# Performance work log

Measured on AMD Instinct MI355X. Metric: run time of the kernel, lower is better.

Reference implementation:

```python
import jax, jax.numpy as jnp
import numpy as np

B, N, H = 32, 2048, 128


def _lstm_step(c, h, x, Wi, Wh, b):
    # flax LSTMCell: gates i,f,g,o; sigmoid/sigmoid/tanh/sigmoid
    gates = x @ Wi + h @ Wh + b  # (B,N,4H)
    i, f, g, o = jnp.split(gates, 4, axis=-1)
    c_new = jax.nn.sigmoid(f) * c + jax.nn.sigmoid(i) * jnp.tanh(g)
    h_new = jax.nn.sigmoid(o) * jnp.tanh(c_new)
    return c_new, h_new


def setup_inputs() -> dict:
    key = jax.random.key(0)
    ks = jax.random.split(key, 24)
    f32 = jnp.float32
    inp = {}
    inp['node_embeddings'] = jax.random.normal(ks[0], (B, N, H), f32)
    for nm, k in zip(['hs_c0', 'hs_h0', 'hs_c1', 'hs_h1'], ks[1:5]):
        inp[nm] = jax.random.normal(k, (B, N, H), f32)
    ip = jax.random.uniform(ks[5], (B, N), f32)
    inp['instruction_pointer'] = ip / jnp.sum(ip, axis=-1, keepdims=True)
    inp['Wi0'] = jax.random.normal(ks[6], (H, 4 * H), f32) * 0.05
    inp['Wh0'] = jax.random.normal(ks[7], (H, 4 * H), f32) * 0.05
    inp['b0'] = jnp.zeros((4 * H,), f32)
    inp['Wi1'] = jax.random.normal(ks[8], (H, 4 * H), f32) * 0.05
    inp['Wh1'] = jax.random.normal(ks[9], (H, 4 * H), f32) * 0.05
    inp['b1'] = jnp.zeros((4 * H,), f32)
    inp['W_raise'] = jax.random.normal(ks[10], (4 * H, 2), f32) * 0.05
    inp['b_raise'] = jnp.zeros((2,), f32)
    inp['W_branch'] = jax.random.normal(ks[11], (4 * H, 2), f32) * 0.05
    inp['b_branch'] = jnp.zeros((2,), f32)
    inp['true_indexes'] = jax.random.randint(ks[12], (B, N), 0, N, jnp.int32)
    inp['false_indexes'] = jax.random.randint(ks[13], (B, N), 0, N, jnp.int32)
    inp['raise_indexes'] = jax.random.randint(ks[14], (B, N), 0, N, jnp.int32)
    inp['exit_node_indexes'] = jax.random.randint(ks[15], (B,), 0, N, jnp.int32)
    inp['raise_node_indexes'] = jax.random.randint(ks[16], (B,), 0, N, jnp.int32)
    inp['step_limits'] = jax.random.randint(ks[17], (B,), 0, 100, jnp.int32)
    inp['current_step'] = 5
    return inp


def reference(node_embeddings, hs_c0, hs_h0, hs_c1, hs_h1, instruction_pointer,
              Wi0, Wh0, b0, Wi1, Wh1, b1, W_raise, b_raise, W_branch, b_branch,
              true_indexes, false_indexes, raise_indexes,
              exit_node_indexes, raise_node_indexes, step_limits, current_step):
    bidx = jnp.arange(B)
    old = [hs_c0, hs_h0, hs_c1, hs_h1]

    # execute: per-node 2-layer stacked LSTM (vectorized over B,N)
    c0n, h0n = _lstm_step(hs_c0, hs_h0, node_embeddings, Wi0, Wh0, b0)
    c1n, h1n = _lstm_step(hs_c1, hs_h1, h0n, Wi1, Wh1, b1)
    contrib = [c0n, h0n, c1n, h1n]

    # mask_h: keep old state at exit node and (raise_in_ipagnn) at raise node
    def mask_nodes(hc, ho, idx):
        return hc.at[bidx, idx].set(ho[bidx, idx])
    contrib = [mask_nodes(mask_nodes(hc, ho, exit_node_indexes), ho, raise_node_indexes)
               for hc, ho in zip(contrib, old)]

    hs_emb = jnp.concatenate(contrib, axis=-1)  # (B,N,4H)

    raise_dec = jax.nn.softmax(hs_emb @ W_raise + b_raise, axis=-1)
    zero_one = jnp.array([0.0, 1.0], dtype=raise_dec.dtype)
    raise_dec = raise_dec.at[bidx, exit_node_indexes].set(zero_one)
    raise_dec = raise_dec.at[bidx, raise_node_indexes].set(zero_one)
    branch_dec = jax.nn.softmax(hs_emb @ W_branch + b_branch, axis=-1)

    p_raise = raise_dec[..., 0]
    p_noraise = raise_dec[..., 1]
    p_true = p_noraise * branch_dec[..., 0]
    p_false = p_noraise * branch_dec[..., 1]

    seg = jax.vmap(lambda v, idx: jax.ops.segment_sum(v, idx, num_segments=N))
    ip = instruction_pointer
    ip_new = (seg(p_raise * ip, raise_indexes)
              + seg(p_true * ip, true_indexes)
              + seg(p_false * ip, false_indexes))  # (B,N)
    denom = (ip_new + 1e-7)[..., None]

    wr = (p_raise * ip)[..., None]
    wt = (p_true * ip)[..., None]
    wf = (p_false * ip)[..., None]

    def agg(h):
        return (seg(h * wr, raise_indexes) + seg(h * wt, true_indexes)
                + seg(h * wf, false_indexes)) / denom
    hs_new = [agg(h) for h in contrib]

    # keep_old_if_done
    not_done = (current_step < step_limits)  # (B,)
    hs_out = [jnp.where(not_done[:, None, None], hn, ho) for hn, ho in zip(hs_new, old)]
    ip_out = jnp.where(not_done[:, None], ip_new, ip)

    # pack carry: (c0,h0,c1,h1, instruction_pointer) -> (B,N,4H+1)
    return jnp.concatenate(hs_out + [ip_out[..., None]], axis=-1)
```

## Files before the change

### kernel.cpp

```cpp
#include <hip/hip_runtime.h>
#include <stdint.h>

#define BB 32
#define NN 2048
#define HH 128
#define BN (BB*NN)

typedef short v8s __attribute__((ext_vector_type(8)));
typedef float v4f __attribute__((ext_vector_type(4)));

__device__ __forceinline__ unsigned short f2b(float f){
  union { float f; unsigned int i; } v; v.f = f;
  unsigned int x = v.i;
  unsigned int r = x + 0x7FFFu + ((x >> 16) & 1u);
  return (unsigned short)(r >> 16);
}
__device__ __forceinline__ unsigned int pk2(float a, float b){
  return (unsigned int)f2b(a) | ((unsigned int)f2b(b) << 16);
}
__device__ __forceinline__ float frcp(float x){ return __builtin_amdgcn_rcpf(x); }
__device__ __forceinline__ float fsigm(float x){ return frcp(1.0f + __expf(-x)); }
__device__ __forceinline__ float ftanh(float x){ return 1.0f - 2.0f*frcp(1.0f + __expf(2.0f*x)); }

__global__ void kswz(const float* __restrict__ Wi0, const float* __restrict__ Wh0,
                     const float* __restrict__ Wi1, const float* __restrict__ Wh1,
                     unsigned short* __restrict__ Bsw0, unsigned short* __restrict__ Bsw1){
  int bid = blockIdx.x;
  int layer = bid >> 8;
  int kc = (bid >> 5) & 7;
  int ct = bid & 31;
  int lane = threadIdx.x;
  const float* Wi = layer ? Wi1 : Wi0;
  const float* Wh = layer ? Wh1 : Wh0;
  unsigned short* dst = layer ? Bsw1 : Bsw0;
  int col = ct*16 + (lane & 15);
  int kbase = kc*32 + (lane >> 4)*8;
  size_t o = ((size_t)(kc*32 + ct)*64 + (size_t)lane)*8;
  #pragma unroll
  for (int j = 0; j < 8; j++){
    int k = kbase + j;
    dst[o + j] = f2b((k < 128) ? Wi[k*512 + col] : Wh[(k-128)*512 + col]);
  }
}

__global__ void ksave(const float* __restrict__ c0, const float* __restrict__ h0,
                      const float* __restrict__ c1, const float* __restrict__ h1,
                      const int* __restrict__ exit_idx, const int* __restrict__ raise_idx,
                      float* __restrict__ saved){
  int b = blockIdx.x, which = blockIdx.y, c = threadIdx.x;
  int idx = which ? raise_idx[b] : exit_idx[b];
  size_t row = (size_t)b*NN + idx;
  const float* bufs[4] = {c0, h0, c1, h1};
  saved[((size_t)b*2 + which)*512 + c] = bufs[c >> 7][row*128 + (c & 127)];
}

__global__ void krestore(float* c0, float* h0, float* c1, float* h1,
                         const int* __restrict__ exit_idx, const int* __restrict__ raise_idx,
                         const float* __restrict__ saved){
  int b = blockIdx.x, which = blockIdx.y, c = threadIdx.x;
  int idx = which ? raise_idx[b] : exit_idx[b];
  size_t row = (size_t)b*NN + idx;
  float* bufs[4] = {c0, h0, c1, h1};
  bufs[c >> 7][row*128 + (c & 127)] = saved[((size_t)b*2 + which)*512 + c];
}

#define ROWSB 32
#define PA 264
#define PH 136

__global__ __launch_bounds__(512, 4) void klstm2(
    const float* __restrict__ ne,
    float* __restrict__ c0, float* __restrict__ h0,
    float* __restrict__ c1, float* __restrict__ h1,
    const unsigned short* __restrict__ Bsw0, const float* __restrict__ b0,
    const unsigned short* __restrict__ Bsw1, const float* __restrict__ b1,
    const int* __restrict__ step_limits, const int* __restrict__ cur_step)
{
  __shared__ unsigned short ldsA[ROWSB*PA];
  __shared__ unsigned short ldsH[ROWSB*PH];
  __shared__ unsigned short ldsG[ROWSB*PH];

  int rowbase = blockIdx.x * ROWSB;
  int b = rowbase >> 11;
  if (cur_step[0] >= step_limits[b]) return;

  int tid = threadIdx.x;
  int wid = tid >> 6, lane = tid & 63;
  int quad = lane >> 4, l16 = lane & 15;
  int ch = wid*16 + l16;

  #pragma unroll
  for (int p = 0; p < 4; p++){
    int idx = p*512 + tid;
    int row = idx >> 6, chunk = idx & 63;
    size_t g = (size_t)(rowbase + row)*128 + (chunk & 31)*4;
    float4 v = (chunk < 32) ? *(const float4*)(ne + g) : *(const float4*)(h0 + g);
    uint2 w; w.x = pk2(v.x, v.y); w.y = pk2(v.z, v.w);
    *(uint2*)&ldsA[row*PA + chunk*4] = w;
  }
  __syncthreads();

  float cpre[8], bias[4];
  #pragma unroll
  for (int rt = 0; rt < 2; rt++)
    #pragma unroll
    for (int r = 0; r < 4; r++)
      cpre[rt*4+r] = c0[((size_t)rowbase + rt*16 + quad*4 + r)*128 + ch];
  #pragma unroll
  for (int g = 0; g < 4; g++) bias[g] = b0[g*128 + ch];

  #pragma unroll
  for (int p = 0; p < 2; p++){
    int idx = p*512 + tid;
    int row = idx >> 5, chunk = idx & 31;
    float4 v = *(const float4*)(h1 + (size_t)(rowbase + row)*128 + chunk*4);
    uint2 w; w.x = pk2(v.x, v.y); w.y = pk2(v.z, v.w);
    *(uint2*)&ldsH[row*PH + chunk*4] = w;
  }

  const v8s* Bv0 = (const v8s*)Bsw0;
  v4f acc[2][4] = {};
  v8s bc[4], bn[4];
  #pragma unroll
  for (int g = 0; g < 4; g++) bc[g] = Bv0[(size_t)(g*8 + wid)*64 + lane];
  #pragma unroll
  for (int kc = 0; kc < 8; kc++){
    if (kc < 7){
      #pragma unroll
      for (int g = 0; g < 4; g++) bn[g] = Bv0[(size_t)((kc+1)*32 + g*8 + wid)*64 + lane];
    }
    v8s a0 = *(const v8s*)&ldsA[(0*16 + l16)*PA + kc*32 + quad*8];
    v8s a1 = *(const v8s*)&ldsA[(1*16 + l16)*PA + kc*32 + quad*8];
    #pragma unroll
    for (int g = 0; g < 4; g++){
      acc[0][g] = __builtin_amdgcn_mfma_f32_16x16x32_bf16(a0, bc[g], acc[0][g], 0,0,0);
      acc[1][g] = __builtin_amdgcn_mfma_f32_16x16x32_bf16(a1, bc[g], acc[1][g], 0,0,0);
    }
    #pragma unroll
    for (int g = 0; g < 4; g++) bc[g] = bn[g];
  }

  #pragma unroll
  for (int rt = 0; rt < 2; rt++){
    #pragma unroll
    for (int r = 0; r < 4; r++){
      int lrow = rt*16 + quad*4 + r;
      size_t row = (size_t)rowbase + lrow;
      float iv = acc[rt][0][r] + bias[0];
      float fv = acc[rt][1][r] + bias[1];
      float gv = acc[rt][2][r] + bias[2];
      float ov = acc[rt][3][r] + bias[3];
      float cold = cpre[rt*4+r];
      float cn = fsigm(fv)*cold + fsigm(iv)*ftanh(gv);
      float hn = fsigm(ov)*ftanh(cn);
      c0[row*128 + ch] = cn;
      h0[row*128 + ch] = hn;
      ldsG[lrow*PH + ch] = f2b(hn);
    }
  }
  __syncthreads();

  #pragma unroll
  for (int rt = 0; rt < 2; rt++)
    #pragma unroll
    for (int r = 0; r < 4; r++)
      cpre[rt*4+r] = c1[((size_t)rowbase + rt*16 + quad*4 + r)*128 + ch];
  #pragma unroll
  for (int g = 0; g < 4; g++) bias[g] = b1[g*128 + ch];

  const v8s* Bv1 = (const v8s*)Bsw1;
  #pragma unroll
  for (int rt = 0; rt < 2; rt++)
    #pragma unroll
    for (int g = 0; g < 4; g++)
      acc[rt][g] = (v4f){0.f, 0.f, 0.f, 0.f};
  #pragma unroll
  for (int g = 0; g < 4; g++) bc[g] = Bv1[(size_t)(g*8 + wid)*64 + lane];
  #pragma unroll
  for (int kc = 0; kc < 8; kc++){
    if (kc < 7){
      #pragma unroll
      for (int g = 0; g < 4; g++) bn[g] = Bv1[(size_t)((kc+1)*32 + g*8 + wid)*64 + lane];
    }
    v8s a0, a1;
    if (kc < 4){
      a0 = *(const v8s*)&ldsG[(0*16 + l16)*PH + kc*32 + quad*8];
      a1 = *(const v8s*)&ldsG[(1*16 + l16)*PH + kc*32 + quad*8];
    } else {
      a0 = *(const v8s*)&ldsH[(0*16 + l16)*PH + (kc-4)*32 + quad*8];
      a1 = *(const v8s*)&ldsH[(1*16 + l16)*PH + (kc-4)*32 + quad*8];
    }
    #pragma unroll
    for (int g = 0; g < 4; g++){
      acc[0][g] = __builtin_amdgcn_mfma_f32_16x16x32_bf16(a0, bc[g], acc[0][g], 0,0,0);
      acc[1][g] = __builtin_amdgcn_mfma_f32_16x16x32_bf16(a1, bc[g], acc[1][g], 0,0,0);
    }
    #pragma unroll
    for (int g = 0; g < 4; g++) bc[g] = bn[g];
  }

  #pragma unroll
  for (int rt = 0; rt < 2; rt++){
    #pragma unroll
    for (int r = 0; r < 4; r++){
      size_t row = (size_t)rowbase + rt*16 + quad*4 + r;
      float iv = acc[rt][0][r] + bias[0];
      float fv = acc[rt][1][r] + bias[1];
      float gv = acc[rt][2][r] + bias[2];
      float ov = acc[rt][3][r] + bias[3];
      float cold = cpre[rt*4+r];
      float cn = fsigm(fv)*cold + fsigm(iv)*ftanh(gv);
      float hn = fsigm(ov)*ftanh(cn);
      c1[row*128 + ch] = cn;
      h1[row*128 + ch] = hn;
    }
  }
}

__global__ __launch_bounds__(256) void kdec(
    const float* __restrict__ c0, const float* __restrict__ h0,
    const float* __restrict__ c1, const float* __restrict__ h1,
    const float* __restrict__ Wr, const float* __restrict__ br,
    const float* __restrict__ Wb, const float* __restrict__ bb,
    const float* __restrict__ ip,
    const int* __restrict__ exit_idx, const int* __restrict__ raise_idx,
    const int* __restrict__ ri, const int* __restrict__ ti, const int* __restrict__ fi,
    int* __restrict__ counts,
    float* __restrict__ wbuf)
{
  int tid = threadIdx.x;
  int wid = tid >> 6, lane = tid & 63;
  int gid = blockIdx.x*4 + wid;
  int b = gid >> 11, n = gid & 2047;

  const float* bufs[4] = {c0, h0, c1, h1};
  const float* hb = bufs[lane >> 4] + (size_t)gid*128 + (lane & 15)*8;
  float4 hv0 = *(const float4*)hb;
  float4 hv1 = *(const float4*)(hb + 4);
  float hv[8] = {hv0.x, hv0.y, hv0.z, hv0.w, hv1.x, hv1.y, hv1.z, hv1.w};
  const float* wrp = Wr + lane*16;
  const float* wbp = Wb + lane*16;
  float r0=0.f, r1=0.f, q0=0.f, q1=0.f;
  #pragma unroll
  for (int j = 0; j < 8; j++){
    float h = hv[j];
    r0 += h * wrp[j*2];  r1 += h * wrp[j*2+1];
    q0 += h * wbp[j*2];  q1 += h * wbp[j*2+1];
  }
  #pragma unroll
  for (int off = 32; off > 0; off >>= 1){
    r0 += __shfl_xor(r0, off, 64);
    r1 += __shfl_xor(r1, off, 64);
    q0 += __shfl_xor(q0, off, 64);
    q1 += __shfl_xor(q1, off, 64);
  }
  if (lane == 0){
    r0 += br[0]; r1 += br[1];
    q0 += bb[0]; q1 += bb[1];
    float pr, pn;
    if (n == exit_idx[b] || n == raise_idx[b]){ pr = 0.f; pn = 1.f; }
    else {
      float m = fmaxf(r0, r1);
      float e0 = __expf(r0 - m), e1 = __expf(r1 - m);
      pr = e0 / (e0 + e1); pn = e1 / (e0 + e1);
    }
    float m2 = fmaxf(q0, q1);
    float f0 = __expf(q0 - m2), f1 = __expf(q1 - m2);
    float pt = f0 / (f0 + f1), pf = f1 / (f0 + f1);
    float ipv = ip[gid];
    wbuf[0*BN + gid] = pr * ipv;
    wbuf[1*BN + gid] = pn * pt * ipv;
    wbuf[2*BN + gid] = pn * pf * ipv;
  } else if (lane == 1){
    atomicAdd(&counts[(b<<11) + ri[gid]], 1);
  } else if (lane == 2){
    atomicAdd(&counts[(b<<11) + ti[gid]], 1);
  } else if (lane == 3){
    atomicAdd(&counts[(b<<11) + fi[gid]], 1);
  }
}

__global__ __launch_bounds__(256) void kscan(const int* __restrict__ counts,
                                             int* __restrict__ offsets){
  __shared__ int lds[256];
  int b = blockIdx.x, tid = threadIdx.x;
  const int* c = counts + b*NN;
  int* o = offsets + b*NN;
  int v[8]; int s = 0;
  #pragma unroll
  for (int i = 0; i < 8; i++){ v[i] = c[tid*8+i]; s += v[i]; }
  lds[tid] = s;
  __syncthreads();
  if (tid == 0){
    int run = 0;
    for (int t = 0; t < 256; t++){ int tmp = lds[t]; lds[t] = run; run += tmp; }
  }
  __syncthreads();
  int off = lds[tid];
  #pragma unroll
  for (int i = 0; i < 8; i++){ o[tid*8+i] = off; off += v[i]; }
}

__global__ void kfill(const int* __restrict__ ri, const int* __restrict__ ti,
                      const int* __restrict__ fi, const int* __restrict__ offsets,
                      int* __restrict__ cursor, unsigned short* __restrict__ edges){
  int gid = blockIdx.x*256 + threadIdx.x;
  int b = gid >> 11, n = gid & 2047;
  size_t ebase = (size_t)b*3*NN;
  int t0 = ri[gid]; int p0 = atomicAdd(&cursor[b*NN+t0], 1);
  edges[ebase + offsets[b*NN+t0] + p0] = (unsigned short)(n);
  int t1 = ti[gid]; int p1 = atomicAdd(&cursor[b*NN+t1], 1);
  edges[ebase + offsets[b*NN+t1] + p1] = (unsigned short)(n | (1<<11));
  int t2 = fi[gid]; int p2 = atomicAdd(&cursor[b*NN+t2], 1);
  edges[ebase + offsets[b*NN+t2] + p2] = (unsigned short)(n | (2<<11));
}

__global__ __launch_bounds__(128) void kagg(
    const float* __restrict__ c0, const float* __restrict__ h0,
    const float* __restrict__ c1, const float* __restrict__ h1,
    const float* __restrict__ ip,
    const float* __restrict__ wbuf, const unsigned short* __restrict__ edges,
    const int* __restrict__ counts, const int* __restrict__ offsets,
    const int* __restrict__ step_limits, const int* __restrict__ cur_step,
    float* __restrict__ out)
{
  int gid = blockIdx.x;
  int b = gid >> 11;
  int tid = threadIdx.x;
  size_t obase = (size_t)gid*513;
  const float* bufs[4] = {c0, h0, c1, h1};

  if (cur_step[0] >= step_limits[b]){
    int c = tid*4;
    const float* s = bufs[c >> 7];
    size_t rb = (size_t)gid*128 + (c & 127);
    out[obase + c+0] = s[rb+0];
    out[obase + c+1] = s[rb+1];
    out[obase + c+2] = s[rb+2];
    out[obase + c+3] = s[rb+3];
    if (tid == 0) out[obase + 512] = ip[gid];
    return;
  }

  int cnt = counts[gid], off = offsets[gid];
  const unsigned short* eb = edges + (size_t)b*3*NN + off;
  const float* sb = bufs[tid >> 5];
  int coff = (tid & 31)*4;
  float a0=0.f, a1=0.f, a2=0.f, a3=0.f, ipn=0.f;
  for (int e = 0; e < cnt; e++){
    int pk = eb[e];
    int n = pk & 2047, et = pk >> 11;
    float w = wbuf[et*BN + (b<<11) + n];
    ipn += w;
    float4 sv = *(const float4*)(sb + ((size_t)(b<<11) + n)*128 + coff);
    a0 += w * sv.x;
    a1 += w * sv.y;
    a2 += w * sv.z;
    a3 += w * sv.w;
  }
  int c = tid*4;
  float inv = 1.0f / (ipn + 1e-7f);
  out[obase + c+0] = a0*inv;
  out[obase + c+1] = a1*inv;
  out[obase + c+2] = a2*inv;
  out[obase + c+3] = a3*inv;
  if (tid == 0) out[obase + 512] = ipn;
}

extern "C" void kernel_launch(void* const* d_in, const int* in_sizes, int n_in,
                              void* d_out, int out_size, void* d_ws, size_t ws_size,
                              hipStream_t stream){
  const float* ne  = (const float*)d_in[0];
  float* c0  = (float*)d_in[1];
  float* h0  = (float*)d_in[2];
  float* c1  = (float*)d_in[3];
  float* h1  = (float*)d_in[4];
  const float* ip  = (const float*)d_in[5];
  const float* Wi0 = (const float*)d_in[6];
  const float* Wh0 = (const float*)d_in[7];
  const float* b0  = (const float*)d_in[8];
  const float* Wi1 = (const float*)d_in[9];
  const float* Wh1 = (const float*)d_in[10];
  const float* b1  = (const float*)d_in[11];
  const float* Wr  = (const float*)d_in[12];
  const float* br  = (const float*)d_in[13];
  const float* Wb  = (const float*)d_in[14];
  const float* bb  = (const float*)d_in[15];
  const int* ti  = (const int*)d_in[16];
  const int* fi  = (const int*)d_in[17];
  const int* ri  = (const int*)d_in[18];
  const int* ei  = (const int*)d_in[19];
  const int* rni = (const int*)d_in[20];
  const int* sl  = (const int*)d_in[21];
  const int* cs  = (const int*)d_in[22];
  float* out = (float*)d_out;

  uint8_t* ws = (uint8_t*)d_ws;
  unsigned short* Bsw0    = (unsigned short*)(ws + 0);
  unsigned short* Bsw1    = (unsigned short*)(ws + 262144);
  float*          saved   = (float*)(ws + 524288);
  float*          wbuf    = (float*)(ws + 655360);
  int*            counts  = (int*)(ws + 1441792);
  int*            offsets = (int*)(ws + 1703936);
  int*            cursor  = (int*)(ws + 1966080);
  unsigned short* edges   = (unsigned short*)(ws + 2228224);

  hipMemsetAsync(counts, 0, BN*sizeof(int), stream);
  hipMemsetAsync(cursor, 0, BN*sizeof(int), stream);

  kswz<<<512, 64, 0, stream>>>(Wi0, Wh0, Wi1, Wh1, Bsw0, Bsw1);
  ksave<<<dim3(BB, 2), 512, 0, stream>>>(c0, h0, c1, h1, ei, rni, saved);

  klstm2<<<BN/ROWSB, 512, 0, stream>>>(ne, c0, h0, c1, h1, Bsw0, b0, Bsw1, b1, sl, cs);

  krestore<<<dim3(BB, 2), 512, 0, stream>>>(c0, h0, c1, h1, ei, rni, saved);

  kdec<<<BN/4, 256, 0, stream>>>(c0, h0, c1, h1, Wr, br, Wb, bb, ip, ei, rni,
                                 ri, ti, fi, counts, wbuf);

  kscan<<<BB, 256, 0, stream>>>(counts, offsets);
  kfill<<<BN/256, 256, 0, stream>>>(ri, ti, fi, offsets, cursor, edges);

  kagg<<<BN, 128, 0, stream>>>(c0, h0, c1, h1, ip, wbuf, edges, counts, offsets,
                               sl, cs, out);
}
```

Baseline: 463.5 us.

## Make LSTM kernel persistent with double-buffered prefetch; drop save/restore kernels and memset

The LSTM kernel becomes a persistent grid of 512 blocks that loops over row tiles. While the current tile computes, it prefetches the next tile's inputs into registers and double-buffered LDS. The exit and raise rows are now skipped in the write-back, so the separate save and restore kernels can be removed. The cursor memset is folded into the scan kernel, and the aggregation loop prefetches the next edge index. This cuts launch count and global-load latency, at the cost of more LDS per block (lower occupancy) and weight fragments reloaded each k-step without the earlier register pipelining.

```diff
diff --git a/kernel.cpp b/kernel.cpp
--- a/kernel.cpp
+++ b/kernel.cpp
@@ -43,28 +43,9 @@
   }
 }
 
-__global__ void ksave(const float* __restrict__ c0, const float* __restrict__ h0,
-                      const float* __restrict__ c1, const float* __restrict__ h1,
-                      const int* __restrict__ exit_idx, const int* __restrict__ raise_idx,
-                      float* __restrict__ saved){
-  int b = blockIdx.x, which = blockIdx.y, c = threadIdx.x;
-  int idx = which ? raise_idx[b] : exit_idx[b];
-  size_t row = (size_t)b*NN + idx;
-  const float* bufs[4] = {c0, h0, c1, h1};
-  saved[((size_t)b*2 + which)*512 + c] = bufs[c >> 7][row*128 + (c & 127)];
-}
-
-__global__ void krestore(float* c0, float* h0, float* c1, float* h1,
-                         const int* __restrict__ exit_idx, const int* __restrict__ raise_idx,
-                         const float* __restrict__ saved){
-  int b = blockIdx.x, which = blockIdx.y, c = threadIdx.x;
-  int idx = which ? raise_idx[b] : exit_idx[b];
-  size_t row = (size_t)b*NN + idx;
-  float* bufs[4] = {c0, h0, c1, h1};
-  bufs[c >> 7][row*128 + (c & 127)] = saved[((size_t)b*2 + which)*512 + c];
-}
-
 #define ROWSB 32
+#define NTILES (BN/ROWSB)
+#define GRID 512
 #define PA 264
 #define PH 136
 
@@ -74,146 +55,205 @@
     float* __restrict__ c1, float* __restrict__ h1,
     const unsigned short* __restrict__ Bsw0, const float* __restrict__ b0,
     const unsigned short* __restrict__ Bsw1, const float* __restrict__ b1,
+    const int* __restrict__ exit_idx, const int* __restrict__ raise_idx,
     const int* __restrict__ step_limits, const int* __restrict__ cur_step)
 {
-  __shared__ unsigned short ldsA[ROWSB*PA];
-  __shared__ unsigned short ldsH[ROWSB*PH];
+  __shared__ unsigned short ldsA[2][ROWSB*PA];
+  __shared__ unsigned short ldsH[2][ROWSB*PH];
   __shared__ unsigned short ldsG[ROWSB*PH];
-
-  int rowbase = blockIdx.x * ROWSB;
-  int b = rowbase >> 11;
-  if (cur_step[0] >= step_limits[b]) return;
 
   int tid = threadIdx.x;
   int wid = tid >> 6, lane = tid & 63;
   int quad = lane >> 4, l16 = lane & 15;
   int ch = wid*16 + l16;
-
-  #pragma unroll
-  for (int p = 0; p < 4; p++){
-    int idx = p*512 + tid;
-    int row = idx >> 6, chunk = idx & 63;
-    size_t g = (size_t)(rowbase + row)*128 + (chunk & 31)*4;
-    float4 v = (chunk < 32) ? *(const float4*)(ne + g) : *(const float4*)(h0 + g);
-    uint2 w; w.x = pk2(v.x, v.y); w.y = pk2(v.z, v.w);
-    *(uint2*)&ldsA[row*PA + chunk*4] = w;
+  int curstep = cur_step[0];
+
+  int arow[4], achk[4], hrow[2], hchk[2];
+  #pragma unroll
+  for (int p = 0; p < 4; p++){ int idx = p*512 + tid; arow[p] = idx >> 6; achk[p] = idx & 63; }
+  #pragma unroll
+  for (int p = 0; p < 2; p++){ int idx = p*512 + tid; hrow[p] = idx >> 5; hchk[p] = idx & 31; }
+
+  const v8s* Bv0 = (const v8s*)Bsw0;
+  const v8s* Bv1 = (const v8s*)Bsw1;
+
+  float4 rgA[4], rgH[2];
+
+  int t0 = blockIdx.x;
+  if (curstep < step_limits[t0 >> 6]){
+    int rowbase = t0 * ROWSB;
+    #pragma unroll
+    for (int p = 0; p < 4; p++){
+      size_t g = (size_t)(rowbase + arow[p])*128 + (achk[p] & 31)*4;
+      rgA[p] = (achk[p] < 32) ? *(const float4*)(ne + g) : *(const float4*)(h0 + g);
+    }
+    #pragma unroll
+    for (int p = 0; p < 2; p++)
+      rgH[p] = *(const float4*)(h1 + (size_t)(rowbase + hrow[p])*128 + hchk[p]*4);
+    #pragma unroll
+    for (int p = 0; p < 4; p++){
+      uint2 w; w.x = pk2(rgA[p].x, rgA[p].y); w.y = pk2(rgA[p].z, rgA[p].w);
+      *(uint2*)&ldsA[0][arow[p]*PA + achk[p]*4] = w;
+    }
+    #pragma unroll
+    for (int p = 0; p < 2; p++){
+      uint2 w; w.x = pk2(rgH[p].x, rgH[p].y); w.y = pk2(rgH[p].z, rgH[p].w);
+      *(uint2*)&ldsH[0][hrow[p]*PH + hchk[p]*4] = w;
+    }
   }
   __syncthreads();
 
-  float cpre[8], bias[4];
-  #pragma unroll
-  for (int rt = 0; rt < 2; rt++)
-    #pragma unroll
-    for (int r = 0; r < 4; r++)
-      cpre[rt*4+r] = c0[((size_t)rowbase + rt*16 + quad*4 + r)*128 + ch];
-  #pragma unroll
-  for (int g = 0; g < 4; g++) bias[g] = b0[g*128 + ch];
-
-  #pragma unroll
-  for (int p = 0; p < 2; p++){
-    int idx = p*512 + tid;
-    int row = idx >> 5, chunk = idx & 31;
-    float4 v = *(const float4*)(h1 + (size_t)(rowbase + row)*128 + chunk*4);
-    uint2 w; w.x = pk2(v.x, v.y); w.y = pk2(v.z, v.w);
-    *(uint2*)&ldsH[row*PH + chunk*4] = w;
-  }
-
-  const v8s* Bv0 = (const v8s*)Bsw0;
-  v4f acc[2][4] = {};
-  v8s bc[4], bn[4];
-  #pragma unroll
-  for (int g = 0; g < 4; g++) bc[g] = Bv0[(size_t)(g*8 + wid)*64 + lane];
-  #pragma unroll
-  for (int kc = 0; kc < 8; kc++){
-    if (kc < 7){
-      #pragma unroll
-      for (int g = 0; g < 4; g++) bn[g] = Bv0[(size_t)((kc+1)*32 + g*8 + wid)*64 + lane];
-    }
-    v8s a0 = *(const v8s*)&ldsA[(0*16 + l16)*PA + kc*32 + quad*8];
-    v8s a1 = *(const v8s*)&ldsA[(1*16 + l16)*PA + kc*32 + quad*8];
-    #pragma unroll
-    for (int g = 0; g < 4; g++){
-      acc[0][g] = __builtin_amdgcn_mfma_f32_16x16x32_bf16(a0, bc[g], acc[0][g], 0,0,0);
-      acc[1][g] = __builtin_amdgcn_mfma_f32_16x16x32_bf16(a1, bc[g], acc[1][g], 0,0,0);
-    }
-    #pragma unroll
-    for (int g = 0; g < 4; g++) bc[g] = bn[g];
-  }
-
-  #pragma unroll
-  for (int rt = 0; rt < 2; rt++){
-    #pragma unroll
-    for (int r = 0; r < 4; r++){
-      int lrow = rt*16 + quad*4 + r;
-      size_t row = (size_t)rowbase + lrow;
-      float iv = acc[rt][0][r] + bias[0];
-      float fv = acc[rt][1][r] + bias[1];
-      float gv = acc[rt][2][r] + bias[2];
-      float ov = acc[rt][3][r] + bias[3];
-      float cold = cpre[rt*4+r];
-      float cn = fsigm(fv)*cold + fsigm(iv)*ftanh(gv);
-      float hn = fsigm(ov)*ftanh(cn);
-      c0[row*128 + ch] = cn;
-      h0[row*128 + ch] = hn;
-      ldsG[lrow*PH + ch] = f2b(hn);
-    }
-  }
-  __syncthreads();
-
-  #pragma unroll
-  for (int rt = 0; rt < 2; rt++)
-    #pragma unroll
-    for (int r = 0; r < 4; r++)
-      cpre[rt*4+r] = c1[((size_t)rowbase + rt*16 + quad*4 + r)*128 + ch];
-  #pragma unroll
-  for (int g = 0; g < 4; g++) bias[g] = b1[g*128 + ch];
-
-  const v8s* Bv1 = (const v8s*)Bsw1;
-  #pragma unroll
-  for (int rt = 0; rt < 2; rt++)
-    #pragma unroll
-    for (int g = 0; g < 4; g++)
-      acc[rt][g] = (v4f){0.f, 0.f, 0.f, 0.f};
-  #pragma unroll
-  for (int g = 0; g < 4; g++) bc[g] = Bv1[(size_t)(g*8 + wid)*64 + lane];
-  #pragma unroll
-  for (int kc = 0; kc < 8; kc++){
-    if (kc < 7){
-      #pragma unroll
-      for (int g = 0; g < 4; g++) bn[g] = Bv1[(size_t)((kc+1)*32 + g*8 + wid)*64 + lane];
-    }
-    v8s a0, a1;
-    if (kc < 4){
-      a0 = *(const v8s*)&ldsG[(0*16 + l16)*PH + kc*32 + quad*8];
-      a1 = *(const v8s*)&ldsG[(1*16 + l16)*PH + kc*32 + quad*8];
-    } else {
-      a0 = *(const v8s*)&ldsH[(0*16 + l16)*PH + (kc-4)*32 + quad*8];
-      a1 = *(const v8s*)&ldsH[(1*16 + l16)*PH + (kc-4)*32 + quad*8];
-    }
-    #pragma unroll
-    for (int g = 0; g < 4; g++){
-      acc[0][g] = __builtin_amdgcn_mfma_f32_16x16x32_bf16(a0, bc[g], acc[0][g], 0,0,0);
-      acc[1][g] = __builtin_amdgcn_mfma_f32_16x16x32_bf16(a1, bc[g], acc[1][g], 0,0,0);
-    }
-    #pragma unroll
-    for (int g = 0; g < 4; g++) bc[g] = bn[g];
-  }
-
-  #pragma unroll
-  for (int rt = 0; rt < 2; rt++){
-    #pragma unroll
-    for (int r = 0; r < 4; r++){
-      size_t row = (size_t)rowbase + rt*16 + quad*4 + r;
-      float iv = acc[rt][0][r] + bias[0];
-      float fv = acc[rt][1][r] + bias[1];
-      float gv = acc[rt][2][r] + bias[2];
-      float ov = acc[rt][3][r] + bias[3];
-      float cold = cpre[rt*4+r];
-      float cn = fsigm(fv)*cold + fsigm(iv)*ftanh(gv);
-      float hn = fsigm(ov)*ftanh(cn);
-      c1[row*128 + ch] = cn;
-      h1[row*128 + ch] = hn;
-    }
+  int cur = 0;
+  for (int t = t0; t < NTILES; t += GRID){
+    int tn = t + GRID;
+    bool alive_c = (curstep < step_limits[t >> 6]);
+    bool alive_n = (tn < NTILES) && (curstep < step_limits[tn >> 6]);
+    int rowbase = t * ROWSB;
+    int b = rowbase >> 11;
+
+    if (alive_n){
+      int rb2 = tn * ROWSB;
+      #pragma unroll
+      for (int p = 0; p < 4; p++){
+        size_t g = (size_t)(rb2 + arow[p])*128 + (achk[p] & 31)*4;
+        rgA[p] = (achk[p] < 32) ? *(const float4*)(ne + g) : *(const float4*)(h0 + g);
+      }
+      #pragma unroll
+      for (int p = 0; p < 2; p++)
+        rgH[p] = *(const float4*)(h1 + (size_t)(rb2 + hrow[p])*128 + hchk[p]*4);
+    }
+
+    v4f acc[2][4] = {};
+    float cpre[8], bias[4];
+    int e_row = 0, r_row = 0;
+
+    if (alive_c){
+      e_row = exit_idx[b]; r_row = raise_idx[b];
+      #pragma unroll
+      for (int rt = 0; rt < 2; rt++)
+        #pragma unroll
+        for (int r = 0; r < 4; r++)
+          cpre[rt*4+r] = c0[((size_t)rowbase + rt*16 + quad*4 + r)*128 + ch];
+      #pragma unroll
+      for (int g = 0; g < 4; g++) bias[g] = b0[g*128 + ch];
+
+      #pragma unroll
+      for (int kc = 0; kc < 8; kc++){
+        v8s f0 = Bv0[(size_t)(kc*32 + 0*8 + wid)*64 + lane];
+        v8s f1 = Bv0[(size_t)(kc*32 + 1*8 + wid)*64 + lane];
+        v8s f2 = Bv0[(size_t)(kc*32 + 2*8 + wid)*64 + lane];
+        v8s f3 = Bv0[(size_t)(kc*32 + 3*8 + wid)*64 + lane];
+        v8s a0 = *(const v8s*)&ldsA[cur][(0*16 + l16)*PA + kc*32 + quad*8];
+        v8s a1 = *(const v8s*)&ldsA[cur][(1*16 + l16)*PA + kc*32 + quad*8];
+        acc[0][0] = __builtin_amdgcn_mfma_f32_16x16x32_bf16(a0, f0, acc[0][0], 0,0,0);
+        acc[1][0] = __builtin_amdgcn_mfma_f32_16x16x32_bf16(a1, f0, acc[1][0], 0,0,0);
+        acc[0][1] = __builtin_amdgcn_mfma_f32_16x16x32_bf16(a0, f1, acc[0][1], 0,0,0);
+        acc[1][1] = __builtin_amdgcn_mfma_f32_16x16x32_bf16(a1, f1, acc[1][1], 0,0,0);
+        acc[0][2] = __builtin_amdgcn_mfma_f32_16x16x32_bf16(a0, f2, acc[0][2], 0,0,0);
+        acc[1][2] = __builtin_amdgcn_mfma_f32_16x16x32_bf16(a1, f2, acc[1][2], 0,0,0);
+        acc[0][3] = __builtin_amdgcn_mfma_f32_16x16x32_bf16(a0, f3, acc[0][3], 0,0,0);
+        acc[1][3] = __builtin_amdgcn_mfma_f32_16x16x32_bf16(a1, f3, acc[1][3], 0,0,0);
+      }
+
+      #pragma unroll
+      for (int rt = 0; rt < 2; rt++){
+        #pragma unroll
+        for (int r = 0; r < 4; r++){
+          int k = rt*4 + r;
+          int lrow = rt*16 + quad*4 + r;
+          int grow = rowbase + lrow;
+          int node = grow & 2047;
+          bool special = (node == e_row) || (node == r_row);
+          float iv = acc[rt][0][r] + bias[0];
+          float fv = acc[rt][1][r] + bias[1];
+          float gv = acc[rt][2][r] + bias[2];
+          float ov = acc[rt][3][r] + bias[3];
+          float cn = fsigm(fv)*cpre[k] + fsigm(iv)*ftanh(gv);
+          float hn = fsigm(ov)*ftanh(cn);
+          if (!special){
+            c0[(size_t)grow*128 + ch] = cn;
+            h0[(size_t)grow*128 + ch] = hn;
+          }
+          ldsG[lrow*PH + ch] = f2b(hn);
+        }
+      }
+
+      #pragma unroll
+      for (int rt = 0; rt < 2; rt++)
+        #pragma unroll
+        for (int r = 0; r < 4; r++)
+          cpre[rt*4+r] = c1[((size_t)rowbase + rt*16 + quad*4 + r)*128 + ch];
+      #pragma unroll
+      for (int g = 0; g < 4; g++) bias[g] = b1[g*128 + ch];
+    }
+    __syncthreads();
+
+    if (alive_c){
+      #pragma unroll
+      for (int rt = 0; rt < 2; rt++)
+        #pragma unroll
+        for (int g = 0; g < 4; g++)
+          acc[rt][g] = (v4f){0.f, 0.f, 0.f, 0.f};
+      #pragma unroll
+      for (int kc = 0; kc < 8; kc++){
+        v8s f0 = Bv1[(size_t)(kc*32 + 0*8 + wid)*64 + lane];
+        v8s f1 = Bv1[(size_t)(kc*32 + 1*8 + wid)*64 + lane];
+        v8s f2 = Bv1[(size_t)(kc*32 + 2*8 + wid)*64 + lane];
+        v8s f3 = Bv1[(size_t)(kc*32 + 3*8 + wid)*64 + lane];
+        v8s a0, a1;
+        if (kc < 4){
+          a0 = *(const v8s*)&ldsG[(0*16 + l16)*PH + kc*32 + quad*8];
+          a1 = *(const v8s*)&ldsG[(1*16 + l16)*PH + kc*32 + quad*8];
+        } else {
+          a0 = *(const v8s*)&ldsH[cur][(0*16 + l16)*PH + (kc-4)*32 + quad*8];
+          a1 = *(const v8s*)&ldsH[cur][(1*16 + l16)*PH + (kc-4)*32 + quad*8];
+        }
+        acc[0][0] = __builtin_amdgcn_mfma_f32_16x16x32_bf16(a0, f0, acc[0][0], 0,0,0);
+        acc[1][0] = __builtin_amdgcn_mfma_f32_16x16x32_bf16(a1, f0, acc[1][0], 0,0,0);
+        acc[0][1] = __builtin_amdgcn_mfma_f32_16x16x32_bf16(a0, f1, acc[0][1], 0,0,0);
+        acc[1][1] = __builtin_amdgcn_mfma_f32_16x16x32_bf16(a1, f1, acc[1][1], 0,0,0);
+        acc[0][2] = __builtin_amdgcn_mfma_f32_16x16x32_bf16(a0, f2, acc[0][2], 0,0,0);
+        acc[1][2] = __builtin_amdgcn_mfma_f32_16x16x32_bf16(a1, f2, acc[1][2], 0,0,0);
+        acc[0][3] = __builtin_amdgcn_mfma_f32_16x16x32_bf16(a0, f3, acc[0][3], 0,0,0);
+        acc[1][3] = __builtin_amdgcn_mfma_f32_16x16x32_bf16(a1, f3, acc[1][3], 0,0,0);
+      }
+
+      #pragma unroll
+      for (int rt = 0; rt < 2; rt++){
+        #pragma unroll
+        for (int r = 0; r < 4; r++){
+          int k = rt*4 + r;
+          int grow = rowbase + rt*16 + quad*4 + r;
+          int node = grow & 2047;
+          bool special = (node == e_row) || (node == r_row);
+          float iv = acc[rt][0][r] + bias[0];
+          float fv = acc[rt][1][r] + bias[1];
+          float gv = acc[rt][2][r] + bias[2];
+          float ov = acc[rt][3][r] + bias[3];
+          float cn = fsigm(fv)*cpre[k] + fsigm(iv)*ftanh(gv);
+          float hn = fsigm(ov)*ftanh(cn);
+          if (!special){
+            c1[(size_t)grow*128 + ch] = cn;
+            h1[(size_t)grow*128 + ch] = hn;
+          }
+        }
+      }
+    }
+
+    if (alive_n){
+      #pragma unroll
+      for (int p = 0; p < 4; p++){
+        uint2 w; w.x = pk2(rgA[p].x, rgA[p].y); w.y = pk2(rgA[p].z, rgA[p].w);
+        *(uint2*)&ldsA[cur^1][arow[p]*PA + achk[p]*4] = w;
+      }
+      #pragma unroll
+      for (int p = 0; p < 2; p++){
+        uint2 w; w.x = pk2(rgH[p].x, rgH[p].y); w.y = pk2(rgH[p].z, rgH[p].w);
+        *(uint2*)&ldsH[cur^1][hrow[p]*PH + hchk[p]*4] = w;
+      }
+    }
+    __syncthreads();
+    cur ^= 1;
   }
 }
 
@@ -281,14 +321,16 @@
 }
 
 __global__ __launch_bounds__(256) void kscan(const int* __restrict__ counts,
-                                             int* __restrict__ offsets){
+                                             int* __restrict__ offsets,
+                                             int* __restrict__ cursor){
   __shared__ int lds[256];
   int b = blockIdx.x, tid = threadIdx.x;
   const int* c = counts + b*NN;
   int* o = offsets + b*NN;
+  int* cu = cursor + b*NN;
   int v[8]; int s = 0;
   #pragma unroll
-  for (int i = 0; i < 8; i++){ v[i] = c[tid*8+i]; s += v[i]; }
+  for (int i = 0; i < 8; i++){ v[i] = c[tid*8+i]; s += v[i]; cu[tid*8+i] = 0; }
   lds[tid] = s;
   __syncthreads();
   if (tid == 0){
@@ -347,16 +389,18 @@
   const float* sb = bufs[tid >> 5];
   int coff = (tid & 31)*4;
   float a0=0.f, a1=0.f, a2=0.f, a3=0.f, ipn=0.f;
+  int pk = (cnt > 0) ? eb[0] : 0;
   for (int e = 0; e < cnt; e++){
-    int pk = eb[e];
+    int pkn = (e+1 < cnt) ? eb[e+1] : 0;
     int n = pk & 2047, et = pk >> 11;
     float w = wbuf[et*BN + (b<<11) + n];
+    float4 sv = *(const float4*)(sb + ((size_t)(b<<11) + n)*128 + coff);
     ipn += w;
-    float4 sv = *(const float4*)(sb + ((size_t)(b<<11) + n)*128 + coff);
     a0 += w * sv.x;
     a1 += w * sv.y;
     a2 += w * sv.z;
     a3 += w * sv.w;
+    pk = pkn;
   }
   int c = tid*4;
   float inv = 1.0f / (ipn + 1e-7f);
@@ -398,7 +442,6 @@
   uint8_t* ws = (uint8_t*)d_ws;
   unsigned short* Bsw0    = (unsigned short*)(ws + 0);
   unsigned short* Bsw1    = (unsigned short*)(ws + 262144);
-  float*          saved   = (float*)(ws + 524288);
   float*          wbuf    = (float*)(ws + 655360);
   int*            counts  = (int*)(ws + 1441792);
   int*            offsets = (int*)(ws + 1703936);
@@ -406,19 +449,16 @@
   unsigned short* edges   = (unsigned short*)(ws + 2228224);
 
   hipMemsetAsync(counts, 0, BN*sizeof(int), stream);
-  hipMemsetAsync(cursor, 0, BN*sizeof(int), stream);
 
   kswz<<<512, 64, 0, stream>>>(Wi0, Wh0, Wi1, Wh1, Bsw0, Bsw1);
-  ksave<<<dim3(BB, 2), 512, 0, stream>>>(c0, h0, c1, h1, ei, rni, saved);
-
-  klstm2<<<BN/ROWSB, 512, 0, stream>>>(ne, c0, h0, c1, h1, Bsw0, b0, Bsw1, b1, sl, cs);
-
-  krestore<<<dim3(BB, 2), 512, 0, stream>>>(c0, h0, c1, h1, ei, rni, saved);
+
+  klstm2<<<GRID, 512, 0, stream>>>(ne, c0, h0, c1, h1, Bsw0, b0, Bsw1, b1,
+                                   ei, rni, sl, cs);
 
   kdec<<<BN/4, 256, 0, stream>>>(c0, h0, c1, h1, Wr, br, Wb, bb, ip, ei, rni,
                                  ri, ti, fi, counts, wbuf);
 
-  kscan<<<BB, 256, 0, stream>>>(counts, offsets);
+  kscan<<<BB, 256, 0, stream>>>(counts, offsets, cursor);
   kfill<<<BN/256, 256, 0, stream>>>(ri, ti, fi, offsets, cursor, edges);
 
   kagg<<<BN, 128, 0, stream>>>(c0, h0, c1, h1, ip, wbuf, edges, counts, offsets,
```

New measurement: 670.0 us. 44.5% more time.
